# Performance work log

Measured on AMD Instinct MI355X. Metric: run time of the kernel, lower is better.

Reference implementation:

```python
import jax, jax.numpy as jnp
import numpy as np

B, C, D_BB, D = 16384, 4, 2048, 512
MAX_NORM = 3.0
LN_EPS = 1e-5


def setup_inputs() -> dict:
    key = jax.random.key(0)
    ks = jax.random.split(key, 6)
    return {
        "thumbnails": jax.random.normal(ks[0], (B, C, D_BB), dtype=jnp.float32),
        # nn.Linear(backbone_dim, hidden_dim): weight [D, D_BB], bias [D]
        "proj_w": jax.random.normal(ks[1], (D, D_BB), dtype=jnp.float32) / np.float32(np.sqrt(D_BB)),
        "proj_b": jnp.zeros((D,), dtype=jnp.float32),
        # per-camera LayerNorm affine params [C, D]
        "gamma": jnp.ones((C, D), dtype=jnp.float32),
        "beta": jnp.zeros((C, D), dtype=jnp.float32),
        # per-camera SwiGLU weights (no bias), torch Linear convention [out, in]
        "w_gate": jax.random.normal(ks[2], (C, D, D), dtype=jnp.float32) / np.float32(np.sqrt(D)),
        "w_val": jax.random.normal(ks[3], (C, D, D), dtype=jnp.float32) / np.float32(np.sqrt(D)),
        # per-camera output proj D->36 (zero-init in module; small random for a useful baseline)
        "w_out": jax.random.normal(ks[4], (C, 36, D), dtype=jnp.float32) * np.float32(0.02),
    }


def _expm66(A):
    """Matrix exponential of [..., 6, 6] matrices with ||A||_F <= MAX_NORM.

    Scaling-and-squaring with a fixed order-12 Taylor series. After scaling by
    2^-4, ||A/16|| <= 0.1875, so the order-12 truncation error is << fp32 eps.
    Matches torch.linalg.matrix_exp to fp32 precision and is fully transposable.
    """
    s = 4  # number of squarings
    As = A * jnp.asarray(1.0 / (2 ** s), A.dtype)
    I = jnp.broadcast_to(jnp.eye(6, dtype=A.dtype), A.shape)
    E = I
    term = I
    for k in range(1, 13):
        term = jnp.matmul(term, As) * jnp.asarray(1.0 / k, A.dtype)
        E = E + term
    for _ in range(s):
        E = jnp.matmul(E, E)
    return E


def reference(thumbnails, proj_w, proj_b, gamma, beta, w_gate, w_val, w_out):
    # thumbnail projection: [B,C,D_BB] @ [D,D_BB]^T -> [B,C,D]
    reg = jnp.einsum('bce,de->bcd', thumbnails, proj_w) + proj_b
    # per-camera LayerNorm (biased variance, as in torch)
    mu = jnp.mean(reg, axis=-1, keepdims=True)
    var = jnp.var(reg, axis=-1, keepdims=True)
    xn = (reg - mu) * jax.lax.rsqrt(var + LN_EPS) * gamma + beta  # gamma/beta broadcast [C,D]
    # SwiGLU (per-camera weights)
    gate = jnp.einsum('bcd,cfd->bcf', xn, w_gate)
    val = jnp.einsum('bcd,cfd->bcf', xn, w_val)
    h = jax.nn.silu(gate) * val
    # project to Lie algebra, skew-symmetrize
    A = jnp.einsum('bcf,cof->bco', h, w_out).reshape(B, C, 6, 6)
    A = A - jnp.swapaxes(A, -1, -2)
    # Frobenius-norm clip to MAX_NORM
    frob = jnp.sqrt(jnp.sum(A * A, axis=(-2, -1), keepdims=True))
    A = A * (jnp.minimum(frob, MAX_NORM) / jnp.maximum(frob, 1e-8))
    # matrix exponential -> orthogonal deltaM, returned as [C, B, 6, 6]
    dM = _expm66(A)
    return jnp.swapaxes(dM, 0, 1)
```

## Files before the change

### kernel.cpp

```cpp
#include <hip/hip_runtime.h>
#include <cstdint>
#include <cstddef>


#define B_SZ   16384
#define C_CAM  4
#define DBB    2048
#define D_H    512

typedef __attribute__((ext_vector_type(8))) short  bf16x8;
typedef __attribute__((ext_vector_type(4))) float  f32x4;

__device__ __forceinline__ unsigned short f2b(float f) {
    union { float f; unsigned u; } v; v.f = f;
    unsigned r = (v.u + 0x7FFFu + ((v.u >> 16) & 1u)) >> 16;
    return (unsigned short)r;
}
__device__ __forceinline__ float b2f(unsigned short u) {
    union { unsigned u; float f; } v; v.u = ((unsigned)u) << 16;
    return v.f;
}

#define GLDS(g, l) __builtin_amdgcn_global_load_lds( \
    (const __attribute__((address_space(1))) unsigned int*)(g), \
    (__attribute__((address_space(3))) unsigned int*)(l), 16, 0, 0)

__global__ void k_cvt(const float* __restrict__ src, unsigned short* __restrict__ dst, int n) {
    int i = blockIdx.x * blockDim.x + threadIdx.x;
    int stride = gridDim.x * blockDim.x;
    for (; i < n; i += stride) dst[i] = f2b(src[i]);
}

__global__ void k_cvt_wout(const float* __restrict__ src, unsigned short* __restrict__ dst) {
    int i = blockIdx.x * blockDim.x + threadIdx.x;
    if (i >= C_CAM * 48 * D_H) return;
    int col = i & (D_H - 1);
    int row = (i >> 9) % 48;
    int c   = i / (48 * D_H);
    dst[i] = (row < 36) ? f2b(src[((size_t)c * 36 + row) * D_H + col]) : (unsigned short)0;
}

__global__ __launch_bounds__(512)
void k_projln(const float* __restrict__ A, const unsigned short* __restrict__ Bw,
              const float* __restrict__ bias, const float* __restrict__ gamma,
              const float* __restrict__ beta, unsigned short* __restrict__ xnb) {
    __shared__ unsigned short lsA[128 * 32];
    __shared__ unsigned short lsB[512 * 32];
    __shared__ float red[2][128][4];

    const int t = threadIdx.x;
    const int tile_m = blockIdx.x * 128;
    const int w = t >> 6, l = t & 63, lr = l & 15, quad = l >> 4;
    const int wm = (w >> 2) * 64;
    const int wn = (w & 3) * 128;

    f32x4 acc[4][8];
#pragma unroll
    for (int i = 0; i < 4; i++)
#pragma unroll
        for (int j = 0; j < 8; j++) acc[i][j] = (f32x4){0.f, 0.f, 0.f, 0.f};

    const int arow = t >> 2, acol = (t & 3) * 8;
    const float* baseA = A + (size_t)(tile_m + arow) * DBB + acol;
    unsigned short* ldsAdst = &lsA[arow * 32 + acol];

    const int srow = l >> 2, scol = (l & 3) * 8;
    const unsigned short* baseB = Bw + (size_t)(w * 64 + srow) * DBB + scol;
    unsigned short* ldsBw = &lsB[w * 64 * 32];

    float4 pa0 = *(const float4*)(baseA);
    float4 pa1 = *(const float4*)(baseA + 4);

    for (int kt = 0; kt < DBB / 32; ++kt) {
        __syncthreads();
        {
            unsigned short o[8] = {f2b(pa0.x), f2b(pa0.y), f2b(pa0.z), f2b(pa0.w),
                                   f2b(pa1.x), f2b(pa1.y), f2b(pa1.z), f2b(pa1.w)};
            *(uint4*)ldsAdst = *(const uint4*)o;
        }
        GLDS(baseB + kt * 32,            ldsBw);
        GLDS(baseB + kt * 32 + 16 * DBB, ldsBw + 16 * 32);
        GLDS(baseB + kt * 32 + 32 * DBB, ldsBw + 32 * 32);
        GLDS(baseB + kt * 32 + 48 * DBB, ldsBw + 48 * 32);
        __syncthreads();

        bf16x8 af[4];
#pragma unroll
        for (int i = 0; i < 4; i++)
            af[i] = *(const bf16x8*)(&lsA[(wm + i * 16 + lr) * 32 + quad * 8]);

        if (kt < DBB / 32 - 1) {
            pa0 = *(const float4*)(baseA + (kt + 1) * 32);
            pa1 = *(const float4*)(baseA + (kt + 1) * 32 + 4);
        }

#pragma unroll
        for (int j = 0; j < 8; j++) {
            const bf16x8 bfr = *(const bf16x8*)(&lsB[(wn + j * 16 + lr) * 32 + quad * 8]);
#pragma unroll
            for (int i = 0; i < 4; i++)
                acc[i][j] = __builtin_amdgcn_mfma_f32_16x16x32_bf16(af[i], bfr, acc[i][j], 0, 0, 0);
        }
    }

#pragma unroll
    for (int j = 0; j < 8; j++) {
        const float bv = bias[wn + j * 16 + lr];
#pragma unroll
        for (int i = 0; i < 4; i++)
#pragma unroll
            for (int r = 0; r < 4; r++) acc[i][j][r] += bv;
    }

    float s[4][4], ss[4][4];
#pragma unroll
    for (int i = 0; i < 4; i++)
#pragma unroll
        for (int r = 0; r < 4; r++) {
            float a = 0.f, b = 0.f;
#pragma unroll
            for (int j = 0; j < 8; j++) { const float x = acc[i][j][r]; a += x; b += x * x; }
            s[i][r] = a; ss[i][r] = b;
        }
#pragma unroll
    for (int off = 1; off <= 8; off <<= 1) {
#pragma unroll
        for (int i = 0; i < 4; i++)
#pragma unroll
            for (int r = 0; r < 4; r++) {
                s[i][r]  += __shfl_xor(s[i][r], off);
                ss[i][r] += __shfl_xor(ss[i][r], off);
            }
    }
    if (lr == 0) {
#pragma unroll
        for (int i = 0; i < 4; i++)
#pragma unroll
            for (int r = 0; r < 4; r++) {
                const int rloc = wm + i * 16 + quad * 4 + r;
                red[0][rloc][w & 3] = s[i][r];
                red[1][rloc][w & 3] = ss[i][r];
            }
    }
    __syncthreads();

    float mu[4][4], rs[4][4];
#pragma unroll
    for (int i = 0; i < 4; i++)
#pragma unroll
        for (int r = 0; r < 4; r++) {
            const int rloc = wm + i * 16 + quad * 4 + r;
            const float S  = red[0][rloc][0] + red[0][rloc][1] + red[0][rloc][2] + red[0][rloc][3];
            const float SS = red[1][rloc][0] + red[1][rloc][1] + red[1][rloc][2] + red[1][rloc][3];
            const float m_ = S * (1.0f / 512.0f);
            const float v_ = SS * (1.0f / 512.0f) - m_ * m_;
            mu[i][r] = m_;
            rs[i][r] = rsqrtf(v_ + 1e-5f);
        }

#pragma unroll
    for (int j = 0; j < 8; j++) {
        const int col = wn + j * 16 + lr;
        float gv[4], bt[4];
#pragma unroll
        for (int r = 0; r < 4; r++) {
            gv[r] = gamma[r * D_H + col];
            bt[r] = beta[r * D_H + col];
        }
#pragma unroll
        for (int i = 0; i < 4; i++) {
            const int bidx = (tile_m + wm + i * 16 + quad * 4) >> 2;
#pragma unroll
            for (int r = 0; r < 4; r++) {
                const float x = (acc[i][j][r] - mu[i][r]) * rs[i][r] * gv[r] + bt[r];
                xnb[((size_t)r * B_SZ + bidx) * D_H + col] = f2b(x);
            }
        }
    }
}

__global__ __launch_bounds__(256)
void k_swiglu(const unsigned short* __restrict__ xnb, const unsigned short* __restrict__ wg,
              const unsigned short* __restrict__ wv, unsigned short* __restrict__ hb) {
    __shared__ unsigned short lsA[128 * 32];
    __shared__ unsigned short lsG[128 * 32];
    __shared__ unsigned short lsV[128 * 32];
    const int t = threadIdx.x;
    const int tile_n = blockIdx.x * 128;
    const int tile_m = blockIdx.y * 128;
    const int cam = blockIdx.z;
    const unsigned short* Ac = xnb + (size_t)cam * B_SZ * D_H;
    const unsigned short* Gc = wg + (size_t)cam * D_H * D_H;
    const unsigned short* Vc = wv + (size_t)cam * D_H * D_H;
    const int w = t >> 6, l = t & 63, lr = l & 15, quad = l >> 4;
    const int wm = (w >> 1) * 64, wn = (w & 1) * 64;

    f32x4 ag[4][4], av[4][4];
#pragma unroll
    for (int i = 0; i < 4; i++)
#pragma unroll
        for (int j = 0; j < 4; j++) { ag[i][j] = (f32x4){0.f,0.f,0.f,0.f}; av[i][j] = (f32x4){0.f,0.f,0.f,0.f}; }

    const int srow = l >> 2, scol = (l & 3) * 8;
    const unsigned short* baseA = Ac + (size_t)(tile_m + w * 32 + srow) * D_H + scol;
    const unsigned short* baseG = Gc + (size_t)(tile_n + w * 32 + srow) * D_H + scol;
    const unsigned short* baseV = Vc + (size_t)(tile_n + w * 32 + srow) * D_H + scol;
    unsigned short* ldsAw = &lsA[w * 32 * 32];
    unsigned short* ldsGw = &lsG[w * 32 * 32];
    unsigned short* ldsVw = &lsV[w * 32 * 32];

    for (int kt = 0; kt < D_H / 32; ++kt) {
        __syncthreads();
        GLDS(baseA + kt * 32,            ldsAw);
        GLDS(baseA + kt * 32 + 16 * D_H, ldsAw + 16 * 32);
        GLDS(baseG + kt * 32,            ldsGw);
        GLDS(baseG + kt * 32 + 16 * D_H, ldsGw + 16 * 32);
        GLDS(baseV + kt * 32,            ldsVw);
        GLDS(baseV + kt * 32 + 16 * D_H, ldsVw + 16 * 32);
        __syncthreads();
        bf16x8 af[4];
#pragma unroll
        for (int i = 0; i < 4; i++)
            af[i] = *(const bf16x8*)(&lsA[(wm + i * 16 + lr) * 32 + quad * 8]);
#pragma unroll
        for (int j = 0; j < 4; j++) {
            bf16x8 gf = *(const bf16x8*)(&lsG[(wn + j * 16 + lr) * 32 + quad * 8]);
            bf16x8 vf = *(const bf16x8*)(&lsV[(wn + j * 16 + lr) * 32 + quad * 8]);
#pragma unroll
            for (int i = 0; i < 4; i++) {
                ag[i][j] = __builtin_amdgcn_mfma_f32_16x16x32_bf16(af[i], gf, ag[i][j], 0, 0, 0);
                av[i][j] = __builtin_amdgcn_mfma_f32_16x16x32_bf16(af[i], vf, av[i][j], 0, 0, 0);
            }
        }
    }
#pragma unroll
    for (int i = 0; i < 4; i++)
#pragma unroll
        for (int j = 0; j < 4; j++)
#pragma unroll
            for (int r = 0; r < 4; r++) {
                const int row = tile_m + wm + i * 16 + quad * 4 + r;
                const int col = tile_n + wn + j * 16 + lr;
                const float g = ag[i][j][r], v = av[i][j][r];
                const float h = g * v / (1.0f + __expf(-g));
                hb[((size_t)cam * B_SZ + row) * D_H + col] = f2b(h);
            }
}

__global__ __launch_bounds__(256)
void k_outproj(const unsigned short* __restrict__ hb, const unsigned short* __restrict__ wo,
               float* __restrict__ Abuf) {
    __shared__ unsigned short lsA[128 * 32];
    __shared__ unsigned short lsB[48 * 32];
    const int t = threadIdx.x;
    const int tile_m = blockIdx.y * 128;
    const int cam = blockIdx.z;
    const unsigned short* Ac = hb + (size_t)cam * B_SZ * D_H;
    const unsigned short* Bc = wo + (size_t)cam * 48 * D_H;
    const int w = t >> 6, l = t & 63, lr = l & 15, quad = l >> 4;
    const int srow = l >> 2, scol = (l & 3) * 8;

    f32x4 acc[2][3];
#pragma unroll
    for (int i = 0; i < 2; i++)
#pragma unroll
        for (int j = 0; j < 3; j++) acc[i][j] = (f32x4){0.f,0.f,0.f,0.f};

    const unsigned short* baseA = Ac + (size_t)(tile_m + w * 32 + srow) * D_H + scol;
    const unsigned short* baseB = Bc + (size_t)(w * 16 + srow) * D_H + scol;
    unsigned short* ldsAw = &lsA[w * 32 * 32];
    unsigned short* ldsBw = &lsB[w * 16 * 32];

    for (int kt = 0; kt < D_H / 32; ++kt) {
        __syncthreads();
        GLDS(baseA + kt * 32,            ldsAw);
        GLDS(baseA + kt * 32 + 16 * D_H, ldsAw + 16 * 32);
        if (w < 3) GLDS(baseB + kt * 32, ldsBw);
        __syncthreads();
        bf16x8 af[2], bfr[3];
#pragma unroll
        for (int i = 0; i < 2; i++)
            af[i] = *(const bf16x8*)(&lsA[(w * 32 + i * 16 + lr) * 32 + quad * 8]);
#pragma unroll
        for (int j = 0; j < 3; j++)
            bfr[j] = *(const bf16x8*)(&lsB[(j * 16 + lr) * 32 + quad * 8]);
#pragma unroll
        for (int i = 0; i < 2; i++)
#pragma unroll
            for (int j = 0; j < 3; j++)
                acc[i][j] = __builtin_amdgcn_mfma_f32_16x16x32_bf16(af[i], bfr[j], acc[i][j], 0, 0, 0);
    }
#pragma unroll
    for (int i = 0; i < 2; i++)
#pragma unroll
        for (int j = 0; j < 3; j++)
#pragma unroll
            for (int r = 0; r < 4; r++) {
                const int col = j * 16 + lr;
                if (col < 36) {
                    const int row = tile_m + w * 32 + i * 16 + quad * 4 + r;
                    Abuf[((size_t)cam * B_SZ + row) * 36 + col] = acc[i][j][r];
                }
            }
}

__global__ __launch_bounds__(128)
void k_expm(const float* __restrict__ Abuf, float* __restrict__ out) {
    const int gid = blockIdx.x * blockDim.x + threadIdx.x;
    if (gid >= B_SZ * C_CAM) return;
    const float* Ap = Abuf + (size_t)gid * 36;

    float a[36];
#pragma unroll
    for (int i = 0; i < 36; i++) a[i] = Ap[i];

    float S[36];
#pragma unroll
    for (int i = 0; i < 6; i++)
#pragma unroll
        for (int j = 0; j < 6; j++) S[i * 6 + j] = a[i * 6 + j] - a[j * 6 + i];

    float fr2 = 0.f;
#pragma unroll
    for (int i = 0; i < 36; i++) fr2 += S[i] * S[i];
    const float fr = sqrtf(fr2);
    const float sc = fminf(fr, 3.0f) / fmaxf(fr, 1e-8f) * 0.0625f;

    float As[36];
#pragma unroll
    for (int i = 0; i < 36; i++) As[i] = S[i] * sc;

    float E[36], T[36], tmp[36];
#pragma unroll
    for (int i = 0; i < 36; i++) { E[i] = (i % 7 == 0) ? 1.f : 0.f; T[i] = E[i]; }

#pragma unroll
    for (int k = 1; k <= 12; k++) {
        const float invk = 1.0f / (float)k;
#pragma unroll
        for (int i = 0; i < 6; i++)
#pragma unroll
            for (int j = 0; j < 6; j++) {
                float sum = 0.f;
#pragma unroll
                for (int q = 0; q < 6; q++) sum += T[i * 6 + q] * As[q * 6 + j];
                tmp[i * 6 + j] = sum * invk;
            }
#pragma unroll
        for (int i = 0; i < 36; i++) { T[i] = tmp[i]; E[i] += tmp[i]; }
    }
#pragma unroll
    for (int sq = 0; sq < 4; sq++) {
#pragma unroll
        for (int i = 0; i < 6; i++)
#pragma unroll
            for (int j = 0; j < 6; j++) {
                float sum = 0.f;
#pragma unroll
                for (int q = 0; q < 6; q++) sum += E[i * 6 + q] * E[q * 6 + j];
                tmp[i * 6 + j] = sum;
            }
#pragma unroll
        for (int i = 0; i < 36; i++) E[i] = tmp[i];
    }

    float* op = out + (size_t)gid * 36;
#pragma unroll
    for (int i = 0; i < 36; i++) op[i] = E[i];
}

extern "C" void kernel_launch(void* const* d_in, const int* in_sizes, int n_in,
                              void* d_out, int out_size, void* d_ws, size_t ws_size,
                              hipStream_t stream) {
    const float* thumb  = (const float*)d_in[0];
    const float* proj_w = (const float*)d_in[1];
    const float* proj_b = (const float*)d_in[2];
    const float* gamma  = (const float*)d_in[3];
    const float* beta   = (const float*)d_in[4];
    const float* w_gate = (const float*)d_in[5];
    const float* w_val  = (const float*)d_in[6];
    const float* w_out  = (const float*)d_in[7];

    char* ws = (char*)d_ws;
    unsigned short* xnb  = (unsigned short*)(ws);
    float*          Abuf = (float*)(ws);
    unsigned short* hb   = (unsigned short*)(ws + 67108864);
    unsigned short* pwb  = (unsigned short*)(ws + 134217728);
    unsigned short* wgb  = (unsigned short*)(ws + 136314880);
    unsigned short* wvb  = (unsigned short*)(ws + 138412032);
    unsigned short* wob  = (unsigned short*)(ws + 140509184);

    hipLaunchKernelGGL(k_cvt, dim3(1024), dim3(256), 0, stream, proj_w, pwb, D_H * DBB);
    hipLaunchKernelGGL(k_cvt, dim3(1024), dim3(256), 0, stream, w_gate, wgb, C_CAM * D_H * D_H);
    hipLaunchKernelGGL(k_cvt, dim3(1024), dim3(256), 0, stream, w_val, wvb, C_CAM * D_H * D_H);
    hipLaunchKernelGGL(k_cvt_wout, dim3((C_CAM * 48 * D_H + 255) / 256), dim3(256), 0, stream, w_out, wob);

    hipLaunchKernelGGL(k_projln, dim3(B_SZ * C_CAM / 128), dim3(512), 0, stream,
                       thumb, pwb, proj_b, gamma, beta, xnb);
    hipLaunchKernelGGL(k_swiglu, dim3(4, 128, 4), dim3(256), 0, stream, xnb, wgb, wvb, hb);
    hipLaunchKernelGGL(k_outproj, dim3(1, 128, 4), dim3(256), 0, stream, hb, wob, Abuf);
    hipLaunchKernelGGL(k_expm, dim3(B_SZ * C_CAM / 128), dim3(128), 0, stream, Abuf, (float*)d_out);
}
```

Baseline: 1.080 ms.

## Fuse SwiGLU and output projection into one kernel; merge weight conversions

```diff
diff --git a/kernel.cpp b/kernel.cpp
--- a/kernel.cpp
+++ b/kernel.cpp
@@ -16,28 +16,37 @@
     unsigned r = (v.u + 0x7FFFu + ((v.u >> 16) & 1u)) >> 16;
     return (unsigned short)r;
 }
-__device__ __forceinline__ float b2f(unsigned short u) {
-    union { unsigned u; float f; } v; v.u = ((unsigned)u) << 16;
-    return v.f;
-}
 
 #define GLDS(g, l) __builtin_amdgcn_global_load_lds( \
     (const __attribute__((address_space(1))) unsigned int*)(g), \
     (__attribute__((address_space(3))) unsigned int*)(l), 16, 0, 0)
 
-__global__ void k_cvt(const float* __restrict__ src, unsigned short* __restrict__ dst, int n) {
-    int i = blockIdx.x * blockDim.x + threadIdx.x;
-    int stride = gridDim.x * blockDim.x;
-    for (; i < n; i += stride) dst[i] = f2b(src[i]);
-}
-
-__global__ void k_cvt_wout(const float* __restrict__ src, unsigned short* __restrict__ dst) {
-    int i = blockIdx.x * blockDim.x + threadIdx.x;
-    if (i >= C_CAM * 48 * D_H) return;
-    int col = i & (D_H - 1);
-    int row = (i >> 9) % 48;
-    int c   = i / (48 * D_H);
-    dst[i] = (row < 36) ? f2b(src[((size_t)c * 36 + row) * D_H + col]) : (unsigned short)0;
+__global__ __launch_bounds__(256)
+void k_cvt_all(const float* __restrict__ proj_w, const float* __restrict__ w_gate,
+               const float* __restrict__ w_val, const float* __restrict__ w_out,
+               unsigned short* __restrict__ pwb, unsigned short* __restrict__ wgb,
+               unsigned short* __restrict__ wvb, unsigned short* __restrict__ wob) {
+    const int idx = blockIdx.x * blockDim.x + threadIdx.x;
+    const int N1 = D_H * DBB;
+    const int N2 = C_CAM * D_H * D_H;
+    if (idx < N1) {
+        pwb[idx] = f2b(proj_w[idx]);
+    } else if (idx < N1 + N2) {
+        const int i = idx - N1;
+        wgb[i] = f2b(w_gate[i]);
+    } else if (idx < N1 + 2 * N2) {
+        const int i = idx - N1 - N2;
+        wvb[i] = f2b(w_val[i]);
+    } else if (idx < N1 + 2 * N2 + C_CAM * 48 * D_H) {
+        const int i = idx - N1 - 2 * N2;
+        const int c = i / (48 * D_H);
+        const int rem = i - c * 48 * D_H;
+        const int row = rem >> 9;
+        const int col = rem & (D_H - 1);
+        const int dcol = col ^ ((row & 7) << 3);
+        wob[c * 48 * D_H + row * D_H + dcol] =
+            (row < 36) ? f2b(w_out[((size_t)c * 36 + row) * D_H + col]) : (unsigned short)0;
+    }
 }
 
 __global__ __launch_bounds__(512)
@@ -179,21 +188,23 @@
     }
 }
 
-__global__ __launch_bounds__(256)
-void k_swiglu(const unsigned short* __restrict__ xnb, const unsigned short* __restrict__ wg,
-              const unsigned short* __restrict__ wv, unsigned short* __restrict__ hb) {
-    __shared__ unsigned short lsA[128 * 32];
-    __shared__ unsigned short lsG[128 * 32];
-    __shared__ unsigned short lsV[128 * 32];
+__global__ __launch_bounds__(512)
+void k_swiglu_out(const unsigned short* __restrict__ xnb, const unsigned short* __restrict__ wg,
+                  const unsigned short* __restrict__ wv, const unsigned short* __restrict__ wo,
+                  float* __restrict__ Abuf) {
+    __shared__ unsigned short lsA[64 * 32];
+    __shared__ unsigned short lsGV[2][512 * 32];
+    __shared__ unsigned short lsO[48 * 512];
+
     const int t = threadIdx.x;
-    const int tile_n = blockIdx.x * 128;
-    const int tile_m = blockIdx.y * 128;
-    const int cam = blockIdx.z;
-    const unsigned short* Ac = xnb + (size_t)cam * B_SZ * D_H;
+    const int tile_m = blockIdx.x * 64;
+    const int cam = blockIdx.y;
+    const unsigned short* Ac = xnb + ((size_t)cam * B_SZ + tile_m) * D_H;
     const unsigned short* Gc = wg + (size_t)cam * D_H * D_H;
     const unsigned short* Vc = wv + (size_t)cam * D_H * D_H;
+    const unsigned short* Oc = wo + (size_t)cam * 48 * D_H;
     const int w = t >> 6, l = t & 63, lr = l & 15, quad = l >> 4;
-    const int wm = (w >> 1) * 64, wn = (w & 1) * 64;
+    const int wn = w * 64;
 
     f32x4 ag[4][4], av[4][4];
 #pragma unroll
@@ -202,30 +213,33 @@
         for (int j = 0; j < 4; j++) { ag[i][j] = (f32x4){0.f,0.f,0.f,0.f}; av[i][j] = (f32x4){0.f,0.f,0.f,0.f}; }
 
     const int srow = l >> 2, scol = (l & 3) * 8;
-    const unsigned short* baseA = Ac + (size_t)(tile_m + w * 32 + srow) * D_H + scol;
-    const unsigned short* baseG = Gc + (size_t)(tile_n + w * 32 + srow) * D_H + scol;
-    const unsigned short* baseV = Vc + (size_t)(tile_n + w * 32 + srow) * D_H + scol;
-    unsigned short* ldsAw = &lsA[w * 32 * 32];
-    unsigned short* ldsGw = &lsG[w * 32 * 32];
-    unsigned short* ldsVw = &lsV[w * 32 * 32];
+    const unsigned short* baseA = Ac + (size_t)((w & 3) * 16 + srow) * D_H + scol;
+    unsigned short* ldsAw = &lsA[(w & 3) * 16 * 32];
+    const unsigned short* baseG = Gc + (size_t)(wn + srow) * D_H + scol;
+    const unsigned short* baseV = Vc + (size_t)(wn + srow) * D_H + scol;
+    unsigned short* ldsGw = &lsGV[0][wn * 32];
+    unsigned short* ldsVw = &lsGV[1][wn * 32];
 
     for (int kt = 0; kt < D_H / 32; ++kt) {
         __syncthreads();
-        GLDS(baseA + kt * 32,            ldsAw);
-        GLDS(baseA + kt * 32 + 16 * D_H, ldsAw + 16 * 32);
+        if (w < 4) GLDS(baseA + kt * 32, ldsAw);
         GLDS(baseG + kt * 32,            ldsGw);
         GLDS(baseG + kt * 32 + 16 * D_H, ldsGw + 16 * 32);
+        GLDS(baseG + kt * 32 + 32 * D_H, ldsGw + 32 * 32);
+        GLDS(baseG + kt * 32 + 48 * D_H, ldsGw + 48 * 32);
         GLDS(baseV + kt * 32,            ldsVw);
         GLDS(baseV + kt * 32 + 16 * D_H, ldsVw + 16 * 32);
+        GLDS(baseV + kt * 32 + 32 * D_H, ldsVw + 32 * 32);
+        GLDS(baseV + kt * 32 + 48 * D_H, ldsVw + 48 * 32);
         __syncthreads();
         bf16x8 af[4];
 #pragma unroll
         for (int i = 0; i < 4; i++)
-            af[i] = *(const bf16x8*)(&lsA[(wm + i * 16 + lr) * 32 + quad * 8]);
+            af[i] = *(const bf16x8*)(&lsA[(i * 16 + lr) * 32 + quad * 8]);
 #pragma unroll
         for (int j = 0; j < 4; j++) {
-            bf16x8 gf = *(const bf16x8*)(&lsG[(wn + j * 16 + lr) * 32 + quad * 8]);
-            bf16x8 vf = *(const bf16x8*)(&lsV[(wn + j * 16 + lr) * 32 + quad * 8]);
+            const bf16x8 gf = *(const bf16x8*)(&lsGV[0][(wn + j * 16 + lr) * 32 + quad * 8]);
+            const bf16x8 vf = *(const bf16x8*)(&lsGV[1][(wn + j * 16 + lr) * 32 + quad * 8]);
 #pragma unroll
             for (int i = 0; i < 4; i++) {
                 ag[i][j] = __builtin_amdgcn_mfma_f32_16x16x32_bf16(af[i], gf, ag[i][j], 0, 0, 0);
@@ -233,75 +247,69 @@
             }
         }
     }
+
+    unsigned short hreg[4][4][4];
 #pragma unroll
     for (int i = 0; i < 4; i++)
 #pragma unroll
         for (int j = 0; j < 4; j++)
 #pragma unroll
             for (int r = 0; r < 4; r++) {
-                const int row = tile_m + wm + i * 16 + quad * 4 + r;
-                const int col = tile_n + wn + j * 16 + lr;
                 const float g = ag[i][j][r], v = av[i][j][r];
-                const float h = g * v / (1.0f + __expf(-g));
-                hb[((size_t)cam * B_SZ + row) * D_H + col] = f2b(h);
-            }
-}
-
-__global__ __launch_bounds__(256)
-void k_outproj(const unsigned short* __restrict__ hb, const unsigned short* __restrict__ wo,
-               float* __restrict__ Abuf) {
-    __shared__ unsigned short lsA[128 * 32];
-    __shared__ unsigned short lsB[48 * 32];
-    const int t = threadIdx.x;
-    const int tile_m = blockIdx.y * 128;
-    const int cam = blockIdx.z;
-    const unsigned short* Ac = hb + (size_t)cam * B_SZ * D_H;
-    const unsigned short* Bc = wo + (size_t)cam * 48 * D_H;
-    const int w = t >> 6, l = t & 63, lr = l & 15, quad = l >> 4;
-    const int srow = l >> 2, scol = (l & 3) * 8;
-
-    f32x4 acc[2][3];
-#pragma unroll
-    for (int i = 0; i < 2; i++)
-#pragma unroll
-        for (int j = 0; j < 3; j++) acc[i][j] = (f32x4){0.f,0.f,0.f,0.f};
-
-    const unsigned short* baseA = Ac + (size_t)(tile_m + w * 32 + srow) * D_H + scol;
-    const unsigned short* baseB = Bc + (size_t)(w * 16 + srow) * D_H + scol;
-    unsigned short* ldsAw = &lsA[w * 32 * 32];
-    unsigned short* ldsBw = &lsB[w * 16 * 32];
-
-    for (int kt = 0; kt < D_H / 32; ++kt) {
-        __syncthreads();
-        GLDS(baseA + kt * 32,            ldsAw);
-        GLDS(baseA + kt * 32 + 16 * D_H, ldsAw + 16 * 32);
-        if (w < 3) GLDS(baseB + kt * 32, ldsBw);
-        __syncthreads();
-        bf16x8 af[2], bfr[3];
-#pragma unroll
-        for (int i = 0; i < 2; i++)
-            af[i] = *(const bf16x8*)(&lsA[(w * 32 + i * 16 + lr) * 32 + quad * 8]);
-#pragma unroll
-        for (int j = 0; j < 3; j++)
-            bfr[j] = *(const bf16x8*)(&lsB[(j * 16 + lr) * 32 + quad * 8]);
-#pragma unroll
-        for (int i = 0; i < 2; i++)
-#pragma unroll
-            for (int j = 0; j < 3; j++)
-                acc[i][j] = __builtin_amdgcn_mfma_f32_16x16x32_bf16(af[i], bfr[j], acc[i][j], 0, 0, 0);
-    }
-#pragma unroll
-    for (int i = 0; i < 2; i++)
+                hreg[i][j][r] = f2b(g * v / (1.0f + __expf(-g)));
+            }
+
+    __syncthreads();
+
+#pragma unroll
+    for (int p = 0; p < 6; p++) {
+        const int inst = w * 6 + p;
+        GLDS(Oc + inst * 512 + l * 8, &lsO[inst * 512]);
+    }
+
+    unsigned short* hls = &lsGV[0][0];
+#pragma unroll
+    for (int i = 0; i < 4; i++)
+#pragma unroll
+        for (int r = 0; r < 4; r++) {
+            const int row = i * 16 + quad * 4 + r;
+            const int sw = (row & 7) << 3;
+#pragma unroll
+            for (int j = 0; j < 4; j++) {
+                const int col = wn + j * 16 + lr;
+                hls[row * D_H + (col ^ sw)] = hreg[i][j][r];
+            }
+        }
+
+    __syncthreads();
+
+    if (w < 4) {
+        f32x4 o[3];
+#pragma unroll
+        for (int j = 0; j < 3; j++) o[j] = (f32x4){0.f,0.f,0.f,0.f};
+        const int arow = w * 16 + lr;
+        const int asw = (arow & 7) << 3;
+#pragma unroll
+        for (int ks = 0; ks < D_H / 32; ++ks) {
+            const bf16x8 af = *(const bf16x8*)(&hls[arow * D_H + ((ks * 32 + quad * 8) ^ asw)]);
+#pragma unroll
+            for (int j = 0; j < 3; j++) {
+                const int brow = j * 16 + lr;
+                const bf16x8 bfr = *(const bf16x8*)(&lsO[brow * D_H + ((ks * 32 + quad * 8) ^ ((brow & 7) << 3))]);
+                o[j] = __builtin_amdgcn_mfma_f32_16x16x32_bf16(af, bfr, o[j], 0, 0, 0);
+            }
+        }
 #pragma unroll
         for (int j = 0; j < 3; j++)
 #pragma unroll
             for (int r = 0; r < 4; r++) {
                 const int col = j * 16 + lr;
                 if (col < 36) {
-                    const int row = tile_m + w * 32 + i * 16 + quad * 4 + r;
-                    Abuf[((size_t)cam * B_SZ + row) * 36 + col] = acc[i][j][r];
+                    const int row = tile_m + w * 16 + quad * 4 + r;
+                    Abuf[((size_t)cam * B_SZ + row) * 36 + col] = o[j][r];
                 }
             }
+    }
 }
 
 __global__ __launch_bounds__(128)
@@ -383,21 +391,19 @@
 
     char* ws = (char*)d_ws;
     unsigned short* xnb  = (unsigned short*)(ws);
-    float*          Abuf = (float*)(ws);
-    unsigned short* hb   = (unsigned short*)(ws + 67108864);
+    float*          Abuf = (float*)(ws + 67108864);
     unsigned short* pwb  = (unsigned short*)(ws + 134217728);
     unsigned short* wgb  = (unsigned short*)(ws + 136314880);
     unsigned short* wvb  = (unsigned short*)(ws + 138412032);
     unsigned short* wob  = (unsigned short*)(ws + 140509184);
 
-    hipLaunchKernelGGL(k_cvt, dim3(1024), dim3(256), 0, stream, proj_w, pwb, D_H * DBB);
-    hipLaunchKernelGGL(k_cvt, dim3(1024), dim3(256), 0, stream, w_gate, wgb, C_CAM * D_H * D_H);
-    hipLaunchKernelGGL(k_cvt, dim3(1024), dim3(256), 0, stream, w_val, wvb, C_CAM * D_H * D_H);
-    hipLaunchKernelGGL(k_cvt_wout, dim3((C_CAM * 48 * D_H + 255) / 256), dim3(256), 0, stream, w_out, wob);
+    const int cvt_total = D_H * DBB + 2 * C_CAM * D_H * D_H + C_CAM * 48 * D_H;
+    hipLaunchKernelGGL(k_cvt_all, dim3((cvt_total + 255) / 256), dim3(256), 0, stream,
+                       proj_w, w_gate, w_val, w_out, pwb, wgb, wvb, wob);
 
     hipLaunchKernelGGL(k_projln, dim3(B_SZ * C_CAM / 128), dim3(512), 0, stream,
                        thumb, pwb, proj_b, gamma, beta, xnb);
-    hipLaunchKernelGGL(k_swiglu, dim3(4, 128, 4), dim3(256), 0, stream, xnb, wgb, wvb, hb);
-    hipLaunchKernelGGL(k_outproj, dim3(1, 128, 4), dim3(256), 0, stream, hb, wob, Abuf);
+    hipLaunchKernelGGL(k_swiglu_out, dim3(B_SZ / 64, C_CAM), dim3(512), 0, stream,
+                       xnb, wgb, wvb, wob, Abuf);
     hipLaunchKernelGGL(k_expm, dim3(B_SZ * C_CAM / 128), dim3(128), 0, stream, Abuf, (float*)d_out);
 }
```

Measured after the change: 1.058 ms. 1.02x faster.
